# Optimization experiments

Measured on AMD Instinct MI355X. Metric: run time of the kernel, lower is better.

The kernel has to match this reference:

```python
import jax, jax.numpy as jnp
import numpy as np

B, D, H, C, T, F = 4096, 1024, 2048, 1000, 819200, 32


def setup_inputs() -> dict:
    key = jax.random.key(0)
    ks = jax.random.split(key, 12)
    feature_vector = jax.random.normal(ks[0], (B, D), dtype=jnp.float32)
    var_flat = jax.random.normal(ks[1], (T, F), dtype=jnp.float32)
    segment_ids = jnp.sort(jax.random.randint(ks[2], (T,), 0, B))
    target_vector = jax.random.randint(ks[3], (B,), 0, C)
    target_scalar = jax.random.normal(ks[4], (B,), dtype=jnp.float32)
    # learned params (torch Linear convention: W [out, in])
    Wv = jax.random.normal(ks[5], (D, F), dtype=jnp.float32) / np.sqrt(F)
    bv = jnp.zeros((D,), dtype=jnp.float32)
    W1 = jax.random.normal(ks[6], (H, D), dtype=jnp.float32) / np.sqrt(D)
    b1 = jnp.zeros((H,), dtype=jnp.float32)
    W2 = jax.random.normal(ks[7], (C, H), dtype=jnp.float32) / np.sqrt(H)
    b2 = jnp.zeros((C,), dtype=jnp.float32)
    Ws = jax.random.normal(ks[8], (1, H), dtype=jnp.float32) / np.sqrt(H)
    bs = jnp.zeros((1,), dtype=jnp.float32)
    return {
        "feature_vector": feature_vector, "var_flat": var_flat,
        "segment_ids": segment_ids, "target_vector": target_vector,
        "target_scalar": target_scalar, "Wv": Wv, "bv": bv,
        "W1": W1, "b1": b1, "W2": W2, "b2": b2, "Ws": Ws, "bs": bs,
    }


def reference(feature_vector, var_flat, segment_ids, target_vector, target_scalar,
              Wv, bv, W1, b1, W2, b2, Ws, bs):
    nb = feature_vector.shape[0]
    # ragged per-item mean via segment reduce (replaces python loop)
    sums = jax.ops.segment_sum(var_flat, segment_ids, num_segments=nb)      # [B, 32]
    counts = jax.ops.segment_sum(jnp.ones((var_flat.shape[0],), var_flat.dtype),
                                 segment_ids, num_segments=nb)
    means = sums / jnp.maximum(counts, 1.0)[:, None]
    var_processed = means @ Wv.T + bv                                        # [B, D]
    combined = feature_vector + var_processed
    hidden = jax.nn.relu(combined @ W1.T + b1)                               # [B, H]
    vector_output = hidden @ W2.T + b2                                       # [B, C]
    scalar_output = (hidden @ Ws.T + bs).squeeze(-1)                         # [B]
    logp = jax.nn.log_softmax(vector_output, axis=-1)
    loss_vector = -jnp.mean(jnp.take_along_axis(logp, target_vector[:, None], axis=1))
    loss_scalar = jnp.mean(jnp.square(scalar_output - target_scalar))
    total_loss = loss_vector + loss_scalar
    acc = jnp.mean((jnp.argmax(vector_output, axis=1) == target_vector).astype(jnp.float32))
    return total_loss, loss_vector, loss_scalar, acc
```

## Files before the change

### kernel.cpp

```cpp
#include <hip/hip_runtime.h>
#include <hip/hip_bf16.h>
#include <math.h>

#define B_  4096
#define D_  1024
#define H_  2048
#define C_  1000
#define T_  819200
#define F_  32
#define NPAD2 1024
#define NPART 1024

typedef __attribute__((ext_vector_type(8))) short short8;
typedef __attribute__((ext_vector_type(4))) float f32x4;

static const size_t WS_MEANS    = 0;
static const size_t WS_PV       = WS_MEANS + (size_t)B_ * F_ * 4;
static const size_t WS_PA       = WS_PV + NPART * 4;
static const size_t WS_PS       = WS_PA + NPART * 4;
static const size_t WS_B2P      = WS_PS + NPART * 4;
static const size_t WS_COMBINED = 1u << 20;
static const size_t WS_W1BF     = WS_COMBINED + (size_t)B_ * D_ * 2;
static const size_t WS_W2BF     = WS_W1BF + (size_t)H_ * D_ * 2;
static const size_t WS_HIDDEN   = WS_W2BF + (size_t)NPAD2 * H_ * 2;
static const size_t WS_LOGITS   = WS_HIDDEN + (size_t)B_ * H_ * 2;

__global__ __launch_bounds__(256) void seg_mean_kernel(
    const float* __restrict__ var_flat, const int* __restrict__ seg_ids,
    float* __restrict__ means) {
  const int seg = blockIdx.x;
  const int tid = threadIdx.x;
  __shared__ int bounds[2];
  if (tid < 2) {
    int tgt = seg + tid;
    int lo = 0, hi = T_;
    while (lo < hi) {
      int mid = (lo + hi) >> 1;
      if (seg_ids[mid] < tgt) lo = mid + 1; else hi = mid;
    }
    bounds[tid] = lo;
  }
  __syncthreads();
  const int start = bounds[0], end = bounds[1];
  const int cnt = end - start;
  const int c4 = (tid & 7) * 4;
  const int rl = tid >> 3;
  float a0 = 0.f, a1 = 0.f, a2 = 0.f, a3 = 0.f;
  for (int r = start + rl; r < end; r += 32) {
    float4 v = *(const float4*)(var_flat + (size_t)r * F_ + c4);
    a0 += v.x; a1 += v.y; a2 += v.z; a3 += v.w;
  }
#pragma unroll
  for (int o = 8; o < 64; o <<= 1) {
    a0 += __shfl_down(a0, o, 64);
    a1 += __shfl_down(a1, o, 64);
    a2 += __shfl_down(a2, o, 64);
    a3 += __shfl_down(a3, o, 64);
  }
  __shared__ float red[4][8][4];
  const int w = tid >> 6, lane = tid & 63;
  if (lane < 8) {
    red[w][lane][0] = a0; red[w][lane][1] = a1;
    red[w][lane][2] = a2; red[w][lane][3] = a3;
  }
  __syncthreads();
  if (tid < 32) {
    int cg = tid >> 2, e = tid & 3;
    float s = red[0][cg][e] + red[1][cg][e] + red[2][cg][e] + red[3][cg][e];
    float inv = cnt > 0 ? 1.f / (float)cnt : 0.f;
    means[(size_t)seg * F_ + cg * 4 + e] = s * inv;
  }
}

__global__ __launch_bounds__(256) void cvt_w1_oct_kernel(
    const float* __restrict__ W1, __hip_bfloat16* __restrict__ dst) {
  int tid = threadIdx.x;
  int d0 = blockIdx.x * 64;
  int n0 = blockIdx.y * 32;
  int n_l = tid >> 3, kc = tid & 7;
  int n = n0 + n_l;
  int dd = d0 + kc * 8;
  float4 a = *(const float4*)(W1 + (size_t)n * D_ + dd);
  float4 b = *(const float4*)(W1 + (size_t)n * D_ + dd + 4);
  __hip_bfloat16 t[8];
  t[0] = __float2bfloat16(a.x); t[1] = __float2bfloat16(a.y);
  t[2] = __float2bfloat16(a.z); t[3] = __float2bfloat16(a.w);
  t[4] = __float2bfloat16(b.x); t[5] = __float2bfloat16(b.y);
  t[6] = __float2bfloat16(b.z); t[7] = __float2bfloat16(b.w);
  *(uint4*)(dst + ((size_t)(blockIdx.x * 8 + kc) * H_ + n) * 8) = *(uint4*)t;
}

__global__ __launch_bounds__(256) void cvt_w2_oct_kernel(
    const float* __restrict__ W2, const float* __restrict__ Ws,
    __hip_bfloat16* __restrict__ dst) {
  int tid = threadIdx.x;
  int h0 = blockIdx.x * 64;
  int n0 = blockIdx.y * 32;
  int n_l = tid >> 3, kc = tid & 7;
  int n = n0 + n_l;
  int hh = h0 + kc * 8;
  float va[8] = {0.f, 0.f, 0.f, 0.f, 0.f, 0.f, 0.f, 0.f};
  const float* src = nullptr;
  if (n < C_)       src = W2 + (size_t)n * H_ + hh;
  else if (n == C_) src = Ws + hh;
  if (src) {
    float4 a = *(const float4*)(src);
    float4 b = *(const float4*)(src + 4);
    va[0] = a.x; va[1] = a.y; va[2] = a.z; va[3] = a.w;
    va[4] = b.x; va[5] = b.y; va[6] = b.z; va[7] = b.w;
  }
  __hip_bfloat16 t[8];
#pragma unroll
  for (int e = 0; e < 8; ++e) t[e] = __float2bfloat16(va[e]);
  *(uint4*)(dst + ((size_t)(blockIdx.x * 8 + kc) * NPAD2 + n) * 8) = *(uint4*)t;
}

__global__ __launch_bounds__(256) void pad_bias_kernel(
    const float* __restrict__ b2, const float* __restrict__ bs,
    float* __restrict__ b2p) {
  int i = blockIdx.x * 256 + threadIdx.x;
  float v = 0.f;
  if (i < C_) v = b2[i];
  else if (i == C_) v = bs[0];
  b2p[i] = v;
}

__global__ __launch_bounds__(256) void combined_kernel(
    const float* __restrict__ feat, const float* __restrict__ means,
    const float* __restrict__ Wv, const float* __restrict__ bv,
    __hip_bfloat16* __restrict__ comb_oct) {
  __shared__ float m_s[32][F_ + 1];
  __shared__ float wv_s[64][F_ + 1];
  int tid = threadIdx.x;
  int d0 = blockIdx.x * 64;
  int b0 = blockIdx.y * 32;
  {
    int b_l = tid >> 3, f4 = (tid & 7) * 4;
    float4 s4 = *(const float4*)(means + (size_t)(b0 + b_l) * F_ + f4);
    m_s[b_l][f4 + 0] = s4.x; m_s[b_l][f4 + 1] = s4.y;
    m_s[b_l][f4 + 2] = s4.z; m_s[b_l][f4 + 3] = s4.w;
  }
  {
    int r = tid >> 2, p = (tid & 3) * 8;
    float4 a = *(const float4*)(Wv + (size_t)(d0 + r) * F_ + p);
    float4 b = *(const float4*)(Wv + (size_t)(d0 + r) * F_ + p + 4);
    wv_s[r][p + 0] = a.x; wv_s[r][p + 1] = a.y; wv_s[r][p + 2] = a.z; wv_s[r][p + 3] = a.w;
    wv_s[r][p + 4] = b.x; wv_s[r][p + 5] = b.y; wv_s[r][p + 6] = b.z; wv_s[r][p + 7] = b.w;
  }
  __syncthreads();
  int b_l = tid >> 3, kc = tid & 7;
  int b = b0 + b_l;
  int dbase = d0 + kc * 8;
  float4 f0 = *(const float4*)(feat + (size_t)b * D_ + dbase);
  float4 f1 = *(const float4*)(feat + (size_t)b * D_ + dbase + 4);
  float4 v0 = *(const float4*)(bv + dbase);
  float4 v1 = *(const float4*)(bv + dbase + 4);
  float fv[8]  = {f0.x, f0.y, f0.z, f0.w, f1.x, f1.y, f1.z, f1.w};
  float bvv[8] = {v0.x, v0.y, v0.z, v0.w, v1.x, v1.y, v1.z, v1.w};
  __hip_bfloat16 outv[8];
#pragma unroll
  for (int e = 0; e < 8; ++e) {
    float acc = fv[e] + bvv[e];
    const float* wr = wv_s[kc * 8 + e];
#pragma unroll
    for (int f = 0; f < F_; ++f) acc = fmaf(m_s[b_l][f], wr[f], acc);
    outv[e] = __float2bfloat16(acc);
  }
  *(uint4*)(comb_oct + ((size_t)(blockIdx.x * 8 + kc) * B_ + b) * 8) = *(uint4*)outv;
}

__device__ inline void load16_lds(const short* g, short* l) {
  __builtin_amdgcn_global_load_lds(
      (const __attribute__((address_space(1))) void*)g,
      (__attribute__((address_space(3))) void*)l, 16, 0, 0);
}

template <int MODE>
__global__ __launch_bounds__(256) void gemm_mfma_kernel(
    const short* __restrict__ A, const short* __restrict__ Bm,
    const float* __restrict__ bias, void* __restrict__ Cout,
    int M, int Nrows, int K, int Nout) {
  __shared__ short As[4][2048];
  __shared__ short Bs[4][4096];
  const int tid  = threadIdx.x;
  const int lane = tid & 63;
  const int w    = tid >> 6;
  const int bm = blockIdx.y * 64;
  const int bn = blockIdx.x * 128;
  const int wm = (w >> 1) * 32;
  const int wn = (w & 1) * 64;
  const int m_lane = lane & 15;
  const int quad   = lane >> 4;

  f32x4 acc[2][4];
#pragma unroll
  for (int i = 0; i < 2; ++i)
#pragma unroll
    for (int j = 0; j < 4; ++j) acc[i][j] = f32x4{0.f, 0.f, 0.f, 0.f};

  const size_t strideA = (size_t)M * 32;
  const size_t strideB = (size_t)Nrows * 32;
  const short* pA  = A  + ((size_t)w * M + bm) * 8 + lane * 8;
  const short* pB0 = Bm + ((size_t)w * Nrows + bn) * 8 + lane * 8;
  const short* pB1 = pB0 + 64 * 8;
  const int lA  = w * 512;
  const int lB0 = w * 1024;
  const int lB1 = lB0 + 512;

#pragma unroll
  for (int s = 0; s < 3; ++s) {
    load16_lds(pA,  &As[s][lA]);
    load16_lds(pB0, &Bs[s][lB0]);
    load16_lds(pB1, &Bs[s][lB1]);
    pA += strideA; pB0 += strideB; pB1 += strideB;
  }

  const int iters = K >> 5;
  for (int it = 0; it < iters; ++it) {
    if (it < iters - 2)       asm volatile("s_waitcnt vmcnt(6)" ::: "memory");
    else if (it == iters - 2) asm volatile("s_waitcnt vmcnt(3)" ::: "memory");
    else                      asm volatile("s_waitcnt vmcnt(0)" ::: "memory");
    asm volatile("s_barrier" ::: "memory");
    if (it + 3 < iters) {
      const int nb = (it + 3) & 3;
      load16_lds(pA,  &As[nb][lA]);
      load16_lds(pB0, &Bs[nb][lB0]);
      load16_lds(pB1, &Bs[nb][lB1]);
      pA += strideA; pB0 += strideB; pB1 += strideB;
    }
    const int cur = it & 3;
    short8 af[2], bf[4];
#pragma unroll
    for (int i = 0; i < 2; ++i)
      af[i] = *(const short8*)&As[cur][quad * 512 + (wm + i * 16 + m_lane) * 8];
#pragma unroll
    for (int j = 0; j < 4; ++j)
      bf[j] = *(const short8*)&Bs[cur][quad * 1024 + (wn + j * 16 + m_lane) * 8];
#pragma unroll
    for (int i = 0; i < 2; ++i)
#pragma unroll
      for (int j = 0; j < 4; ++j)
        acc[i][j] = __builtin_amdgcn_mfma_f32_16x16x32_bf16(af[i], bf[j], acc[i][j], 0, 0, 0);
  }

  const int row0 = bm + wm + quad * 4;
  const int col0 = bn + wn + m_lane;
  if (MODE == 0) {
    __hip_bfloat16* Cb = (__hip_bfloat16*)Cout;
#pragma unroll
    for (int j = 0; j < 4; ++j) {
      int col = col0 + j * 16;
      float bsv = bias[col];
      __hip_bfloat16* base = Cb + ((size_t)(col >> 3) * M) * 8 + (col & 7);
#pragma unroll
      for (int i = 0; i < 2; ++i)
#pragma unroll
        for (int r = 0; r < 4; ++r) {
          int row = row0 + i * 16 + r;
          float v = acc[i][j][r] + bsv;
          v = v > 0.f ? v : 0.f;
          base[(size_t)row * 8] = __float2bfloat16(v);
        }
    }
  } else {
    float* Cf = (float*)Cout;
#pragma unroll
    for (int j = 0; j < 4; ++j) {
      int col = col0 + j * 16;
      float bsv = bias[col];
#pragma unroll
      for (int i = 0; i < 2; ++i)
#pragma unroll
        for (int r = 0; r < 4; ++r) {
          int row = row0 + i * 16 + r;
          Cf[(size_t)row * Nout + col] = acc[i][j][r] + bsv;
        }
    }
  }
}

__global__ __launch_bounds__(256) void loss_kernel(
    const float* __restrict__ logits, const int* __restrict__ target,
    const float* __restrict__ tgt_scal,
    float* __restrict__ pv, float* __restrict__ pa, float* __restrict__ ps) {
  int tid  = threadIdx.x;
  int lane = tid & 63;
  int w    = tid >> 6;
  int b    = blockIdx.x * 4 + w;
  const float*  row  = logits + (size_t)b * NPAD2;
  const float4* row4 = (const float4*)row;
  float v[16];
  float vmax = -INFINITY;
  int   imax = 0x7fffffff;
#pragma unroll
  for (int k = 0; k < 4; ++k) {
    int c4 = lane + 64 * k;
    float4 x = row4[c4];
    float e0 = x.x, e1 = x.y, e2 = x.z, e3 = x.w;
    int idx = c4 * 4;
    if (idx + 0 >= C_) e0 = -INFINITY;
    if (idx + 1 >= C_) e1 = -INFINITY;
    if (idx + 2 >= C_) e2 = -INFINITY;
    if (idx + 3 >= C_) e3 = -INFINITY;
    v[k * 4 + 0] = e0; v[k * 4 + 1] = e1; v[k * 4 + 2] = e2; v[k * 4 + 3] = e3;
    if (e0 > vmax) { vmax = e0; imax = idx + 0; }
    if (e1 > vmax) { vmax = e1; imax = idx + 1; }
    if (e2 > vmax) { vmax = e2; imax = idx + 2; }
    if (e3 > vmax) { vmax = e3; imax = idx + 3; }
  }
#pragma unroll
  for (int o = 32; o > 0; o >>= 1) {
    float ov = __shfl_down(vmax, o, 64);
    int   oi = __shfl_down(imax, o, 64);
    if (ov > vmax || (ov == vmax && oi < imax)) { vmax = ov; imax = oi; }
  }
  vmax = __shfl(vmax, 0, 64);
  float se = 0.f;
#pragma unroll
  for (int j = 0; j < 16; ++j) se += expf(v[j] - vmax);
#pragma unroll
  for (int o = 32; o > 0; o >>= 1) se += __shfl_down(se, o, 64);
  __shared__ float s_nll[4], s_acc[4], s_sq[4];
  if (lane == 0) {
    int t = target[b];
    float logp = row[t] - vmax - logf(se);
    s_nll[w] = -logp;
    s_acc[w] = (imax == t) ? 1.f : 0.f;
    float d = row[C_] - tgt_scal[b];
    s_sq[w] = d * d;
  }
  __syncthreads();
  if (tid == 0) {
    pv[blockIdx.x] = s_nll[0] + s_nll[1] + s_nll[2] + s_nll[3];
    pa[blockIdx.x] = s_acc[0] + s_acc[1] + s_acc[2] + s_acc[3];
    ps[blockIdx.x] = s_sq[0] + s_sq[1] + s_sq[2] + s_sq[3];
  }
}

__global__ __launch_bounds__(256) void finalize_kernel(
    const float* __restrict__ pv, const float* __restrict__ pa,
    const float* __restrict__ ps, float* __restrict__ out) {
  int tid  = threadIdx.x;
  int lane = tid & 63;
  int w    = tid >> 6;
  float nll = 0.f, acc = 0.f, sq = 0.f;
  for (int i = tid; i < NPART; i += 256) {
    nll += pv[i]; acc += pa[i]; sq += ps[i];
  }
#pragma unroll
  for (int o = 32; o > 0; o >>= 1) {
    nll += __shfl_down(nll, o, 64);
    acc += __shfl_down(acc, o, 64);
    sq  += __shfl_down(sq,  o, 64);
  }
  __shared__ float sn[4], sa[4], ss[4];
  if (lane == 0) { sn[w] = nll; sa[w] = acc; ss[w] = sq; }
  __syncthreads();
  if (tid == 0) {
    float lv = (sn[0] + sn[1] + sn[2] + sn[3]) * (1.f / B_);
    float ls = (ss[0] + ss[1] + ss[2] + ss[3]) * (1.f / B_);
    float ac = (sa[0] + sa[1] + sa[2] + sa[3]) * (1.f / B_);
    out[0] = lv + ls;
    out[1] = lv;
    out[2] = ls;
    out[3] = ac;
  }
}

extern "C" void kernel_launch(void* const* d_in, const int* in_sizes, int n_in,
                              void* d_out, int out_size, void* d_ws, size_t ws_size,
                              hipStream_t stream) {
  const float* feature  = (const float*)d_in[0];
  const float* var_flat = (const float*)d_in[1];
  const int*   seg_ids  = (const int*)d_in[2];
  const int*   tgt_vec  = (const int*)d_in[3];
  const float* tgt_scal = (const float*)d_in[4];
  const float* Wv = (const float*)d_in[5];
  const float* bv = (const float*)d_in[6];
  const float* W1 = (const float*)d_in[7];
  const float* b1 = (const float*)d_in[8];
  const float* W2 = (const float*)d_in[9];
  const float* b2 = (const float*)d_in[10];
  const float* Ws = (const float*)d_in[11];
  const float* bs = (const float*)d_in[12];
  float* out = (float*)d_out;

  char* ws = (char*)d_ws;
  float* means  = (float*)(ws + WS_MEANS);
  float* pv     = (float*)(ws + WS_PV);
  float* pa     = (float*)(ws + WS_PA);
  float* ps     = (float*)(ws + WS_PS);
  float* b2p    = (float*)(ws + WS_B2P);
  __hip_bfloat16* comb_oct = (__hip_bfloat16*)(ws + WS_COMBINED);
  __hip_bfloat16* W1oct    = (__hip_bfloat16*)(ws + WS_W1BF);
  __hip_bfloat16* W2oct    = (__hip_bfloat16*)(ws + WS_W2BF);
  __hip_bfloat16* hid_oct  = (__hip_bfloat16*)(ws + WS_HIDDEN);
  float*          logits   = (float*)(ws + WS_LOGITS);

  seg_mean_kernel<<<B_, 256, 0, stream>>>(var_flat, seg_ids, means);

  {
    dim3 g1(D_ / 64, H_ / 32);
    cvt_w1_oct_kernel<<<g1, 256, 0, stream>>>(W1, W1oct);
    dim3 g2(H_ / 64, NPAD2 / 32);
    cvt_w2_oct_kernel<<<g2, 256, 0, stream>>>(W2, Ws, W2oct);
    pad_bias_kernel<<<NPAD2 / 256, 256, 0, stream>>>(b2, bs, b2p);
  }

  {
    dim3 grid(D_ / 64, B_ / 32);
    combined_kernel<<<grid, 256, 0, stream>>>(feature, means, Wv, bv, comb_oct);
  }

  {
    dim3 grid(H_ / 128, B_ / 64);
    gemm_mfma_kernel<0><<<grid, 256, 0, stream>>>(
        (const short*)comb_oct, (const short*)W1oct, b1, hid_oct, B_, H_, D_, H_);
  }

  {
    dim3 grid(NPAD2 / 128, B_ / 64);
    gemm_mfma_kernel<1><<<grid, 256, 0, stream>>>(
        (const short*)hid_oct, (const short*)W2oct, b2p, logits, B_, NPAD2, H_, NPAD2);
  }

  loss_kernel<<<B_ / 4, 256, 0, stream>>>(logits, tgt_vec, tgt_scal, pv, pa, ps);

  finalize_kernel<<<1, 256, 0, stream>>>(pv, pa, ps, out);
}
```

Measured before the change: 314.3 us.

## Fuse prep kernels into one launch and use double-buffered GEMM pipeline

Merges the segment-mean, W1/W2 bf16 conversion and bias padding kernels into a single prep kernel that dispatches on block index, removing three launches. The MFMA GEMM drops from a 4-stage LDS ring with hand-tuned vmcnt waits to a 2-stage double buffer synchronised with __syncthreads. This halves LDS use per block, which may allow more resident blocks per CU. In exchange, fewer loads are kept in flight, so memory latency is hidden less within each block.

```diff
diff --git a/kernel.cpp b/kernel.cpp
--- a/kernel.cpp
+++ b/kernel.cpp
@@ -25,104 +25,112 @@
 static const size_t WS_HIDDEN   = WS_W2BF + (size_t)NPAD2 * H_ * 2;
 static const size_t WS_LOGITS   = WS_HIDDEN + (size_t)B_ * H_ * 2;
 
-__global__ __launch_bounds__(256) void seg_mean_kernel(
+#define PREP_BLOCKS (B_ + 1024 + 1024 + 4)
+__global__ __launch_bounds__(256) void prep_kernel(
     const float* __restrict__ var_flat, const int* __restrict__ seg_ids,
-    float* __restrict__ means) {
-  const int seg = blockIdx.x;
+    float* __restrict__ means,
+    const float* __restrict__ W1, __hip_bfloat16* __restrict__ W1oct,
+    const float* __restrict__ W2, const float* __restrict__ Wsc,
+    __hip_bfloat16* __restrict__ W2oct,
+    const float* __restrict__ b2, const float* __restrict__ bsc,
+    float* __restrict__ b2p) {
+  const int id  = blockIdx.x;
   const int tid = threadIdx.x;
-  __shared__ int bounds[2];
-  if (tid < 2) {
-    int tgt = seg + tid;
-    int lo = 0, hi = T_;
-    while (lo < hi) {
-      int mid = (lo + hi) >> 1;
-      if (seg_ids[mid] < tgt) lo = mid + 1; else hi = mid;
-    }
-    bounds[tid] = lo;
-  }
-  __syncthreads();
-  const int start = bounds[0], end = bounds[1];
-  const int cnt = end - start;
-  const int c4 = (tid & 7) * 4;
-  const int rl = tid >> 3;
-  float a0 = 0.f, a1 = 0.f, a2 = 0.f, a3 = 0.f;
-  for (int r = start + rl; r < end; r += 32) {
-    float4 v = *(const float4*)(var_flat + (size_t)r * F_ + c4);
-    a0 += v.x; a1 += v.y; a2 += v.z; a3 += v.w;
-  }
-#pragma unroll
-  for (int o = 8; o < 64; o <<= 1) {
-    a0 += __shfl_down(a0, o, 64);
-    a1 += __shfl_down(a1, o, 64);
-    a2 += __shfl_down(a2, o, 64);
-    a3 += __shfl_down(a3, o, 64);
-  }
-  __shared__ float red[4][8][4];
-  const int w = tid >> 6, lane = tid & 63;
-  if (lane < 8) {
-    red[w][lane][0] = a0; red[w][lane][1] = a1;
-    red[w][lane][2] = a2; red[w][lane][3] = a3;
-  }
-  __syncthreads();
-  if (tid < 32) {
-    int cg = tid >> 2, e = tid & 3;
-    float s = red[0][cg][e] + red[1][cg][e] + red[2][cg][e] + red[3][cg][e];
-    float inv = cnt > 0 ? 1.f / (float)cnt : 0.f;
-    means[(size_t)seg * F_ + cg * 4 + e] = s * inv;
-  }
-}
-
-__global__ __launch_bounds__(256) void cvt_w1_oct_kernel(
-    const float* __restrict__ W1, __hip_bfloat16* __restrict__ dst) {
-  int tid = threadIdx.x;
-  int d0 = blockIdx.x * 64;
-  int n0 = blockIdx.y * 32;
-  int n_l = tid >> 3, kc = tid & 7;
-  int n = n0 + n_l;
-  int dd = d0 + kc * 8;
-  float4 a = *(const float4*)(W1 + (size_t)n * D_ + dd);
-  float4 b = *(const float4*)(W1 + (size_t)n * D_ + dd + 4);
-  __hip_bfloat16 t[8];
-  t[0] = __float2bfloat16(a.x); t[1] = __float2bfloat16(a.y);
-  t[2] = __float2bfloat16(a.z); t[3] = __float2bfloat16(a.w);
-  t[4] = __float2bfloat16(b.x); t[5] = __float2bfloat16(b.y);
-  t[6] = __float2bfloat16(b.z); t[7] = __float2bfloat16(b.w);
-  *(uint4*)(dst + ((size_t)(blockIdx.x * 8 + kc) * H_ + n) * 8) = *(uint4*)t;
-}
-
-__global__ __launch_bounds__(256) void cvt_w2_oct_kernel(
-    const float* __restrict__ W2, const float* __restrict__ Ws,
-    __hip_bfloat16* __restrict__ dst) {
-  int tid = threadIdx.x;
-  int h0 = blockIdx.x * 64;
-  int n0 = blockIdx.y * 32;
-  int n_l = tid >> 3, kc = tid & 7;
-  int n = n0 + n_l;
-  int hh = h0 + kc * 8;
-  float va[8] = {0.f, 0.f, 0.f, 0.f, 0.f, 0.f, 0.f, 0.f};
-  const float* src = nullptr;
-  if (n < C_)       src = W2 + (size_t)n * H_ + hh;
-  else if (n == C_) src = Ws + hh;
-  if (src) {
-    float4 a = *(const float4*)(src);
-    float4 b = *(const float4*)(src + 4);
-    va[0] = a.x; va[1] = a.y; va[2] = a.z; va[3] = a.w;
-    va[4] = b.x; va[5] = b.y; va[6] = b.z; va[7] = b.w;
-  }
-  __hip_bfloat16 t[8];
-#pragma unroll
-  for (int e = 0; e < 8; ++e) t[e] = __float2bfloat16(va[e]);
-  *(uint4*)(dst + ((size_t)(blockIdx.x * 8 + kc) * NPAD2 + n) * 8) = *(uint4*)t;
-}
-
-__global__ __launch_bounds__(256) void pad_bias_kernel(
-    const float* __restrict__ b2, const float* __restrict__ bs,
-    float* __restrict__ b2p) {
-  int i = blockIdx.x * 256 + threadIdx.x;
-  float v = 0.f;
-  if (i < C_) v = b2[i];
-  else if (i == C_) v = bs[0];
-  b2p[i] = v;
+
+  if (id < B_) {
+    const int seg = id;
+    __shared__ int bounds[2];
+    __shared__ float red[4][8][4];
+    if (tid < 2) {
+      int tgt = seg + tid;
+      int lo = 0, hi = T_;
+      while (lo < hi) {
+        int mid = (lo + hi) >> 1;
+        if (seg_ids[mid] < tgt) lo = mid + 1; else hi = mid;
+      }
+      bounds[tid] = lo;
+    }
+    __syncthreads();
+    const int start = bounds[0], end = bounds[1];
+    const int cnt = end - start;
+    const int c4 = (tid & 7) * 4;
+    const int rl = tid >> 3;
+    float a0 = 0.f, a1 = 0.f, a2 = 0.f, a3 = 0.f;
+    for (int r = start + rl; r < end; r += 32) {
+      float4 v = *(const float4*)(var_flat + (size_t)r * F_ + c4);
+      a0 += v.x; a1 += v.y; a2 += v.z; a3 += v.w;
+    }
+#pragma unroll
+    for (int o = 8; o < 64; o <<= 1) {
+      a0 += __shfl_down(a0, o, 64);
+      a1 += __shfl_down(a1, o, 64);
+      a2 += __shfl_down(a2, o, 64);
+      a3 += __shfl_down(a3, o, 64);
+    }
+    const int w = tid >> 6, lane = tid & 63;
+    if (lane < 8) {
+      red[w][lane][0] = a0; red[w][lane][1] = a1;
+      red[w][lane][2] = a2; red[w][lane][3] = a3;
+    }
+    __syncthreads();
+    if (tid < 32) {
+      int cg = tid >> 2, e = tid & 3;
+      float s = red[0][cg][e] + red[1][cg][e] + red[2][cg][e] + red[3][cg][e];
+      float inv = cnt > 0 ? 1.f / (float)cnt : 0.f;
+      means[(size_t)seg * F_ + cg * 4 + e] = s * inv;
+    }
+    return;
+  }
+
+  if (id < B_ + 1024) {
+    int t = id - B_;
+    int bx = t & 15, by = t >> 4;
+    int d0 = bx * 64, n0 = by * 32;
+    int n_l = tid >> 3, kc = tid & 7;
+    int n = n0 + n_l;
+    int dd = d0 + kc * 8;
+    float4 a = *(const float4*)(W1 + (size_t)n * D_ + dd);
+    float4 b = *(const float4*)(W1 + (size_t)n * D_ + dd + 4);
+    __hip_bfloat16 tb[8];
+    tb[0] = __float2bfloat16(a.x); tb[1] = __float2bfloat16(a.y);
+    tb[2] = __float2bfloat16(a.z); tb[3] = __float2bfloat16(a.w);
+    tb[4] = __float2bfloat16(b.x); tb[5] = __float2bfloat16(b.y);
+    tb[6] = __float2bfloat16(b.z); tb[7] = __float2bfloat16(b.w);
+    *(uint4*)(W1oct + ((size_t)(bx * 8 + kc) * H_ + n) * 8) = *(uint4*)tb;
+    return;
+  }
+
+  if (id < B_ + 2048) {
+    int t = id - B_ - 1024;
+    int bx = t & 31, by = t >> 5;
+    int h0 = bx * 64, n0 = by * 32;
+    int n_l = tid >> 3, kc = tid & 7;
+    int n = n0 + n_l;
+    int hh = h0 + kc * 8;
+    float va[8] = {0.f, 0.f, 0.f, 0.f, 0.f, 0.f, 0.f, 0.f};
+    const float* src = nullptr;
+    if (n < C_)       src = W2 + (size_t)n * H_ + hh;
+    else if (n == C_) src = Wsc + hh;
+    if (src) {
+      float4 a = *(const float4*)(src);
+      float4 b = *(const float4*)(src + 4);
+      va[0] = a.x; va[1] = a.y; va[2] = a.z; va[3] = a.w;
+      va[4] = b.x; va[5] = b.y; va[6] = b.z; va[7] = b.w;
+    }
+    __hip_bfloat16 tb[8];
+#pragma unroll
+    for (int e = 0; e < 8; ++e) tb[e] = __float2bfloat16(va[e]);
+    *(uint4*)(W2oct + ((size_t)(bx * 8 + kc) * NPAD2 + n) * 8) = *(uint4*)tb;
+    return;
+  }
+
+  {
+    int i = (id - B_ - 2048) * 256 + tid;
+    float v = 0.f;
+    if (i < C_) v = b2[i];
+    else if (i == C_) v = bsc[0];
+    b2p[i] = v;
+  }
 }
 
 __global__ __launch_bounds__(256) void combined_kernel(
@@ -180,8 +188,8 @@
     const short* __restrict__ A, const short* __restrict__ Bm,
     const float* __restrict__ bias, void* __restrict__ Cout,
     int M, int Nrows, int K, int Nout) {
-  __shared__ short As[4][2048];
-  __shared__ short Bs[4][4096];
+  __shared__ short As[2][2048];
+  __shared__ short Bs[2][4096];
   const int tid  = threadIdx.x;
   const int lane = tid & 63;
   const int w    = tid >> 6;
@@ -207,28 +215,20 @@
   const int lB0 = w * 1024;
   const int lB1 = lB0 + 512;
 
-#pragma unroll
-  for (int s = 0; s < 3; ++s) {
-    load16_lds(pA,  &As[s][lA]);
-    load16_lds(pB0, &Bs[s][lB0]);
-    load16_lds(pB1, &Bs[s][lB1]);
-    pA += strideA; pB0 += strideB; pB1 += strideB;
-  }
+  load16_lds(pA,  &As[0][lA]);
+  load16_lds(pB0, &Bs[0][lB0]);
+  load16_lds(pB1, &Bs[0][lB1]);
 
   const int iters = K >> 5;
   for (int it = 0; it < iters; ++it) {
-    if (it < iters - 2)       asm volatile("s_waitcnt vmcnt(6)" ::: "memory");
-    else if (it == iters - 2) asm volatile("s_waitcnt vmcnt(3)" ::: "memory");
-    else                      asm volatile("s_waitcnt vmcnt(0)" ::: "memory");
-    asm volatile("s_barrier" ::: "memory");
-    if (it + 3 < iters) {
-      const int nb = (it + 3) & 3;
-      load16_lds(pA,  &As[nb][lA]);
-      load16_lds(pB0, &Bs[nb][lB0]);
-      load16_lds(pB1, &Bs[nb][lB1]);
+    const int cur = it & 1, nxt = cur ^ 1;
+    __syncthreads();
+    if (it + 1 < iters) {
       pA += strideA; pB0 += strideB; pB1 += strideB;
-    }
-    const int cur = it & 3;
+      load16_lds(pA,  &As[nxt][lA]);
+      load16_lds(pB0, &Bs[nxt][lB0]);
+      load16_lds(pB1, &Bs[nxt][lB1]);
+    }
     short8 af[2], bf[4];
 #pragma unroll
     for (int i = 0; i < 2; ++i)
@@ -397,15 +397,8 @@
   __hip_bfloat16* hid_oct  = (__hip_bfloat16*)(ws + WS_HIDDEN);
   float*          logits   = (float*)(ws + WS_LOGITS);
 
-  seg_mean_kernel<<<B_, 256, 0, stream>>>(var_flat, seg_ids, means);
-
-  {
-    dim3 g1(D_ / 64, H_ / 32);
-    cvt_w1_oct_kernel<<<g1, 256, 0, stream>>>(W1, W1oct);
-    dim3 g2(H_ / 64, NPAD2 / 32);
-    cvt_w2_oct_kernel<<<g2, 256, 0, stream>>>(W2, Ws, W2oct);
-    pad_bias_kernel<<<NPAD2 / 256, 256, 0, stream>>>(b2, bs, b2p);
-  }
+  prep_kernel<<<PREP_BLOCKS, 256, 0, stream>>>(
+      var_flat, seg_ids, means, W1, W1oct, W2, Ws, W2oct, b2, bs, b2p);
 
   {
     dim3 grid(D_ / 64, B_ / 32);
```

Measured after the change: 295.4 us. 1.06x faster.
